# Kernel optimization log

Measured on AMD Instinct MI355X. Metric: run time of the kernel, lower is better.

## Reference

```python
import jax, jax.numpy as jnp
import numpy as np
from jax import lax


def setup_inputs() -> dict:
    key = jax.random.key(0)
    B, S, C = 64, 4096, 128
    timeseries = jax.random.normal(key, (B, S, C), dtype=jnp.float32)
    return {"timeseries": timeseries, "k": 64}


def reference(timeseries, k):
    B, S, C = timeseries.shape
    ffts = jnp.fft.rfft(timeseries, axis=1)          # (B, F, C) complex, F = S//2 + 1
    F = ffts.shape[1]
    mags = jnp.abs(ffts)                              # (B, F, C)
    # top-k magnitudes per (batch, channel): move freq axis last for lax.top_k
    m = jnp.transpose(mags, (0, 2, 1))                # (B, C, F)
    _, idx = lax.top_k(m, k)                          # (B, C, k)
    mask = jnp.zeros((B, C, F), dtype=bool)
    mask = mask.at[jnp.arange(B)[:, None, None],
                   jnp.arange(C)[None, :, None],
                   idx].set(True)
    mask = jnp.transpose(mask, (0, 2, 1))             # (B, F, C)
    filtered = jnp.where(mask, ffts, jnp.zeros((), dtype=ffts.dtype))
    reconstructed = jnp.fft.irfft(filtered, n=S, axis=1)  # (B, S, C) real
    return reconstructed.astype(timeseries.dtype)
```

## Files before the change

### kernel.cpp

```cpp
#include <hip/hip_runtime.h>
#include <math.h>

#define TPB 256
#define SWZ(i) ((i) ^ (((i) >> 5) & 31) ^ ((i) >> 10))

#define A2048 0.0030679615757712823f
#define A256  0.0245436926061702596f
#define A32   0.1963495408493620774f
#define APACK 0.0015339807878856411f
#define EPSB  1.220703125e-4f

__device__ __forceinline__ float2 cadd(float2 a, float2 b){return make_float2(a.x+b.x, a.y+b.y);}
__device__ __forceinline__ float2 csub(float2 a, float2 b){return make_float2(a.x-b.x, a.y-b.y);}
__device__ __forceinline__ float2 cmul(float2 a, float2 b){return make_float2(a.x*b.x-a.y*b.y, a.x*b.y+a.y*b.x);}
__device__ __forceinline__ float2 cni(float2 a){return make_float2(a.y, -a.x);}
__device__ __forceinline__ float2 cpi(float2 a){return make_float2(-a.y, a.x);}

__device__ __forceinline__ int pos2048(int k) {
  return 256*(k&7) + 32*((k>>3)&7) + 4*((k>>6)&7) + ((k>>9)&3);
}

__device__ __forceinline__ void fft8(float2 y[8]) {
  const float S2 = 0.70710678118654752f;
  float2 B0=cadd(y[0],y[4]), B4=csub(y[0],y[4]);
  float2 B1=cadd(y[1],y[5]), B5=csub(y[1],y[5]);
  float2 B2=cadd(y[2],y[6]), B6=csub(y[2],y[6]);
  float2 B3=cadd(y[3],y[7]), B7=csub(y[3],y[7]);
  float2 C0=cadd(B0,B2), C2=csub(B0,B2);
  float2 C1=cadd(B1,B3), C3=csub(B1,B3);
  float2 n6=cni(B6), n7=cni(B7);
  float2 C4=cadd(B4,n6), C6=csub(B4,n6);
  float2 C5=cadd(B5,n7), C7=csub(B5,n7);
  y[0]=cadd(C0,C1); y[4]=csub(C0,C1);
  float2 n3=cni(C3);
  y[2]=cadd(C2,n3); y[6]=csub(C2,n3);
  float2 t5=make_float2(S2*(C5.x+C5.y), S2*(C5.y-C5.x));
  y[1]=cadd(C4,t5); y[5]=csub(C4,t5);
  float2 t7=make_float2(S2*(C7.y-C7.x), -S2*(C7.x+C7.y));
  y[3]=cadd(C6,t7); y[7]=csub(C6,t7);
}

__device__ __forceinline__ void ifft8(float2 y[8]) {
  const float S2 = 0.70710678118654752f;
  float2 B0=cadd(y[0],y[4]), B4=csub(y[0],y[4]);
  float2 B1=cadd(y[1],y[5]), B5=csub(y[1],y[5]);
  float2 B2=cadd(y[2],y[6]), B6=csub(y[2],y[6]);
  float2 B3=cadd(y[3],y[7]), B7=csub(y[3],y[7]);
  float2 C0=cadd(B0,B2), C2=csub(B0,B2);
  float2 C1=cadd(B1,B3), C3=csub(B1,B3);
  float2 p6=cpi(B6), p7=cpi(B7);
  float2 C4=cadd(B4,p6), C6=csub(B4,p6);
  float2 C5=cadd(B5,p7), C7=csub(B5,p7);
  y[0]=cadd(C0,C1); y[4]=csub(C0,C1);
  float2 p3=cpi(C3);
  y[2]=cadd(C2,p3); y[6]=csub(C2,p3);
  float2 t5=make_float2(S2*(C5.x-C5.y), S2*(C5.x+C5.y));
  y[1]=cadd(C4,t5); y[5]=csub(C4,t5);
  float2 t7=make_float2(-S2*(C7.x+C7.y), S2*(C7.x-C7.y));
  y[3]=cadd(C6,t7); y[7]=csub(C6,t7);
}

__device__ __forceinline__ void r8stage(float2* Zf, int idx0, int st, float a1, bool inv) {
  float2 y[8];
#pragma unroll
  for (int s=0;s<8;++s) y[s]=Zf[SWZ(idx0+st*s)];
  float sn, cs; __sincosf(a1, &sn, &cs);
  float2 w1=make_float2(cs,sn);
  float2 w2=cmul(w1,w1), w3=cmul(w2,w1), w4=cmul(w2,w2);
  float2 w5=cmul(w4,w1), w6=cmul(w4,w2), w7=cmul(w4,w3);
  if (inv){
    y[1]=cmul(y[1],w1); y[2]=cmul(y[2],w2); y[3]=cmul(y[3],w3);
    y[4]=cmul(y[4],w4); y[5]=cmul(y[5],w5); y[6]=cmul(y[6],w6); y[7]=cmul(y[7],w7);
    ifft8(y);
  } else {
    fft8(y);
    y[1]=cmul(y[1],w1); y[2]=cmul(y[2],w2); y[3]=cmul(y[3],w3);
    y[4]=cmul(y[4],w4); y[5]=cmul(y[5],w5); y[6]=cmul(y[6],w6); y[7]=cmul(y[7],w7);
  }
#pragma unroll
  for (int s=0;s<8;++s) Zf[SWZ(idx0+st*s)] = y[s];
}

__global__ __launch_bounds__(256) void tposeX(const float* __restrict__ in,
                                              float* __restrict__ out,
                                              int R, int Cd, int lgx) {
  __shared__ float tile[64][65];
  int t = threadIdx.x;
  int q = t & 15, r = t >> 4;
  int id = blockIdx.x;
  int g = id & 7, j = id >> 3;
  int w = ((j >> 3) << 6) | (g << 3) | (j & 7);
  int b = w >> 7;
  int rem = w & 127;
  int gxm = (1 << lgx) - 1;
  int c0 = (rem & gxm) * 64, r0 = (rem >> lgx) * 64;
  const float4* in4 = reinterpret_cast<const float4*>(in + (size_t)b * R * Cd);
  float4* out4 = reinterpret_cast<float4*>(out + (size_t)b * R * Cd);
#pragma unroll
  for (int rr = r; rr < 64; rr += 16) {
    float4 v = in4[((size_t)(r0 + rr) * Cd + c0) / 4 + q];
    tile[rr][4 * q + 0] = v.x; tile[rr][4 * q + 1] = v.y;
    tile[rr][4 * q + 2] = v.z; tile[rr][4 * q + 3] = v.w;
  }
  __syncthreads();
#pragma unroll
  for (int cc = r; cc < 64; cc += 16) {
    float4 wv;
    wv.x = tile[4 * q + 0][cc]; wv.y = tile[4 * q + 1][cc];
    wv.z = tile[4 * q + 2][cc]; wv.w = tile[4 * q + 3][cc];
    out4[((size_t)(c0 + cc) * R + r0) / 4 + q] = wv;
  }
}

__global__ __launch_bounds__(TPB, 6) void fourier_topk_kernel(
    const float* __restrict__ src, float* __restrict__ dst,
    const int* __restrict__ kptr, int strideT) {
  __shared__ float2 Zf[2048];
  __shared__ unsigned int histL[1056];
  __shared__ unsigned char maskA[2052];
  __shared__ int tieIdx[64];
  __shared__ double candV[64];
  __shared__ double cpR[4], cpI[4];
  __shared__ unsigned int bcD, bcR, bcCnt, bcT, bcG, bcTieN;

  const int tid = threadIdx.x;
  int i = blockIdx.x;
  int xj = i & 7, mm = i >> 3;
  int c = 16 * xj + (mm & 15);
  int b = mm >> 4;
  const size_t base = (strideT == 1) ? ((size_t)(b * 128 + c)) * 4096
                                     : ((size_t)b * 4096 * 128 + (size_t)c);
  const float* sp = src + base;
  float* dp = dst + base;

  if (strideT == 1) {
    const float4* sp4 = reinterpret_cast<const float4*>(sp);
#pragma unroll
    for (int it = 0; it < 4; ++it) {
      int t4 = tid + 256 * it;
      float4 v = sp4[t4];
      Zf[SWZ(2*t4)]   = make_float2(v.x, v.y);
      Zf[SWZ(2*t4+1)] = make_float2(v.z, v.w);
    }
  } else {
#pragma unroll
    for (int it = 0; it < 8; ++it) {
      int n = tid + 256 * it;
      float a = sp[(size_t)(2*n) * strideT];
      float bb = sp[(size_t)(2*n+1) * strideT];
      Zf[SWZ(n)] = make_float2(a, bb);
    }
  }
  __syncthreads();

  r8stage(Zf, tid, 256, -A2048 * (float)tid, false);
  __syncthreads();
  r8stage(Zf, 256*(tid>>5) + (tid&31), 32, -A256 * (float)(tid&31), false);
  __syncthreads();
  r8stage(Zf, 32*(tid>>2) + (tid&3), 4, -A32 * (float)(tid&3), false);
  __syncthreads();
#pragma unroll
  for (int h = 0; h < 2; ++h) {
    int i0 = 4 * (tid + 256*h);
    float2 A0=Zf[SWZ(i0)], A1=Zf[SWZ(i0+1)], A2=Zf[SWZ(i0+2)], A3=Zf[SWZ(i0+3)];
    float2 f=cadd(A0,A2), e=csub(A0,A2), g=cadd(A1,A3), d=csub(A1,A3);
    float2 nd=cni(d);
    Zf[SWZ(i0)]   = cadd(f,g);
    Zf[SWZ(i0+1)] = cadd(e,nd);
    Zf[SWZ(i0+2)] = csub(f,g);
    Zf[SWZ(i0+3)] = csub(e,nd);
  }
  __syncthreads();

  float kA[4], kB[4];
#pragma unroll
  for (int jj = 0; jj < 4; ++jj) {
    int k = tid + 256 * jj;
    float2 za = Zf[SWZ(pos2048(k))];
    float2 zb = Zf[SWZ(pos2048((2048 - k) & 2047))];
    float her = 0.5f*(za.x+zb.x), hei = 0.5f*(za.y-zb.y);
    float hor = 0.5f*(za.y+zb.y), hoi = -0.5f*(za.x-zb.x);
    float sn, cs; __sincosf(-APACK * (float)k, &sn, &cs);
    float whr = cs*hor - sn*hoi, whi = cs*hoi + sn*hor;
    float x1r = her + whr, x1i = hei + whi;
    float x2r = her - whr, x2i = whi - hei;
    kA[jj] = x1r*x1r + x1i*x1i;
    kB[jj] = x2r*x2r + x2i*x2i;
  }
  float kNy;
  {
    float2 za = Zf[SWZ(pos2048(1024))];
    kNy = za.x*za.x + za.y*za.y;
  }
  const bool hasNy = (tid == 0);

  int kk = kptr[0];
  if (kk > 2049) kk = 2049;
  if (kk < 1) kk = 1;
  unsigned int prefix = 0u, pmask = 0u, Tkey = 0u;
  bool haveT = false;
  int R = kk;
  unsigned int* myh = &histL[(tid >> 6) * 264];
#pragma unroll 1
  for (int p = 0; p < 4; ++p) {
    if (!haveT) {
      const int sh = 24 - 8 * p;
      for (int idx2 = tid; idx2 < 1056; idx2 += TPB) histL[idx2] = 0u;
      __syncthreads();
#pragma unroll
      for (int jj = 0; jj < 4; ++jj) {
        unsigned int u = __float_as_uint(kA[jj]);
        if ((u & pmask) == prefix) atomicAdd(&myh[(u >> sh) & 255u], 1u);
        u = __float_as_uint(kB[jj]);
        if ((u & pmask) == prefix) atomicAdd(&myh[(u >> sh) & 255u], 1u);
      }
      if (hasNy) {
        unsigned int u = __float_as_uint(kNy);
        if ((u & pmask) == prefix) atomicAdd(&myh[(u >> sh) & 255u], 1u);
      }
      __syncthreads();
      if (tid < 64) {
        int L = tid;
        int s0 = 0, s1 = 0, s2 = 0, s3 = 0;
#pragma unroll
        for (int wv = 0; wv < 4; ++wv) {
          const unsigned int* hw = &histL[wv * 264];
          s0 += (int)hw[4*L]; s1 += (int)hw[4*L+1];
          s2 += (int)hw[4*L+2]; s3 += (int)hw[4*L+3];
        }
        int loc = s0 + s1 + s2 + s3;
        int suf = loc;
#pragma unroll
        for (int off = 1; off < 64; off <<= 1) {
          int tt = __shfl(suf, (L + off) & 63, 64);
          suf += (L + off < 64) ? tt : 0;
        }
        int e3 = suf - loc, i3 = e3 + s3;
        int e2 = i3,        i2 = e2 + s2;
        int e1 = i2,        i1 = e1 + s1;
        int e0 = i1,        i0 = e0 + s0;
        if (e3 < R && R <= i3) { bcD = 4*L+3; bcR = R - e3; bcCnt = s3; }
        if (e2 < R && R <= i2) { bcD = 4*L+2; bcR = R - e2; bcCnt = s2; }
        if (e1 < R && R <= i1) { bcD = 4*L+1; bcR = R - e1; bcCnt = s1; }
        if (e0 < R && R <= i0) { bcD = 4*L+0; bcR = R - e0; bcCnt = s0; }
      }
      __syncthreads();
      prefix |= (bcD << sh);
      pmask |= (255u << sh);
      R = (int)bcR;
      if (bcCnt == 1u) {
#pragma unroll
        for (int jj = 0; jj < 4; ++jj) {
          unsigned int u = __float_as_uint(kA[jj]);
          if ((u & pmask) == prefix) bcT = u;
          u = __float_as_uint(kB[jj]);
          if ((u & pmask) == prefix) bcT = u;
        }
        if (hasNy) {
          unsigned int u = __float_as_uint(kNy);
          if ((u & pmask) == prefix) bcT = u;
        }
        __syncthreads();
        Tkey = bcT;
        haveT = true;
      }
      __syncthreads();
    }
  }
  if (!haveT) Tkey = prefix;

  float Tf = __uint_as_float(Tkey);
  float Thi = Tf * (1.0f + EPSB), Tlo = Tf * (1.0f - EPSB);
  if (tid == 0) { bcG = 0u; bcTieN = 0u; }
  __syncthreads();
#pragma unroll
  for (int jj = 0; jj < 4; ++jj) {
    float v = kA[jj];
    if (v > Thi) atomicAdd(&bcG, 1u);
    else if (v >= Tlo) {
      int pos = (int)atomicAdd(&bcTieN, 1u);
      if (pos < 64) tieIdx[pos] = tid + 256 * jj;
    }
    v = kB[jj];
    if (v > Thi) atomicAdd(&bcG, 1u);
    else if (v >= Tlo) {
      int pos = (int)atomicAdd(&bcTieN, 1u);
      if (pos < 64) tieIdx[pos] = 2048 - (tid + 256 * jj);
    }
  }
  if (hasNy) {
    if (kNy > Thi) atomicAdd(&bcG, 1u);
    else if (kNy >= Tlo) {
      int pos = (int)atomicAdd(&bcTieN, 1u);
      if (pos < 64) tieIdx[pos] = 1024;
    }
  }
  __syncthreads();
  int G = (int)bcG, E = (int)bcTieN, need = kk - G;

  if (need >= E) {
#pragma unroll
    for (int jj = 0; jj < 4; ++jj) {
      int k = tid + 256 * jj;
      maskA[k]        = (kA[jj] >= Tlo) ? 1 : 0;
      maskA[2048 - k] = (kB[jj] >= Tlo) ? 1 : 0;
    }
    if (hasNy) maskA[1024] = (kNy >= Tlo) ? 1 : 0;
    __syncthreads();
  } else {
#pragma unroll
    for (int jj = 0; jj < 4; ++jj) {
      int k = tid + 256 * jj;
      maskA[k]        = (kA[jj] > Thi) ? 1 : 0;
      maskA[2048 - k] = (kB[jj] > Thi) ? 1 : 0;
    }
    if (hasNy) maskA[1024] = (kNy > Thi) ? 1 : 0;
    __syncthreads();
    int nt = E < 64 ? E : 64;
    for (int ci = 0; ci < nt; ++ci) {
      int kq = tieIdx[ci];
      double sr = 0.0, si = 0.0;
#pragma unroll 1
      for (int j = 0; j < 16; ++j) {
        int m = tid + 256 * j;
        double xm = (double)sp[(size_t)m * strideT];
        int a = (kq * m) & 4095;
        double ang = 1.5339807878856412e-3 * (double)a;
        double sv, cv; sincos(ang, &sv, &cv);
        sr += xm * cv; si -= xm * sv;
      }
#pragma unroll
      for (int off = 1; off < 64; off <<= 1) {
        sr += __shfl_xor(sr, off); si += __shfl_xor(si, off);
      }
      if ((tid & 63) == 0) { cpR[tid >> 6] = sr; cpI[tid >> 6] = si; }
      __syncthreads();
      if (tid == 0) {
        double Rr = cpR[0]+cpR[1]+cpR[2]+cpR[3];
        double Ii = cpI[0]+cpI[1]+cpI[2]+cpI[3];
        candV[ci] = Rr*Rr + Ii*Ii;
      }
      __syncthreads();
    }
    if (tid == 0) {
      unsigned char* ch = (unsigned char*)histL;
      for (int t = 0; t < nt; ++t) ch[t] = 0;
      int lim = need < nt ? need : nt;
      for (int s = 0; s < lim; ++s) {
        int best = -1;
        for (int t = 0; t < nt; ++t) {
          if (ch[t]) continue;
          if (best < 0 || candV[t] > candV[best] ||
              (candV[t] == candV[best] && tieIdx[t] < tieIdx[best])) best = t;
        }
        if (best >= 0) { ch[best] = 1; maskA[tieIdx[best]] = 1; }
      }
    }
    __syncthreads();
  }

#pragma unroll
  for (int jj = 0; jj < 4; ++jj) {
    int k = tid + 256 * jj;
    if (k == 0) {
      int p0 = SWZ(pos2048(0));
      float2 z0 = Zf[p0];
      float X0 = z0.x + z0.y, XN = z0.x - z0.y;
      float A = maskA[0] ? X0 : 0.0f, Bv = maskA[2048] ? XN : 0.0f;
      Zf[p0] = make_float2(0.5f*(A + Bv), 0.5f*(A - Bv));
      int p1 = SWZ(pos2048(1024));
      float2 z1 = Zf[p1];
      float m1 = maskA[1024] ? 1.0f : 0.0f;
      Zf[p1] = make_float2(m1 * z1.x, m1 * z1.y);
    } else {
      int pa = SWZ(pos2048(k)), pb = SWZ(pos2048(2048 - k));
      float2 za = Zf[pa], zb = Zf[pb];
      float her = 0.5f*(za.x+zb.x), hei = 0.5f*(za.y-zb.y);
      float hor = 0.5f*(za.y+zb.y), hoi = -0.5f*(za.x-zb.x);
      float sn, cs; __sincosf(-APACK * (float)k, &sn, &cs);
      float wr = cs, wi = sn;
      float whr = wr*hor - wi*hoi, whi = wr*hoi + wi*hor;
      float x1r = her + whr, x1i = hei + whi;
      float x2r = her - whr, x2i = whi - hei;
      float mA = maskA[k] ? 1.0f : 0.0f, mB = maskA[2048 - k] ? 1.0f : 0.0f;
      float Ar = mA*x1r, Ai = mA*x1i, Br = mB*x2r, Bi = mB*x2i;
      float sr = Ar + Br, si = Ai - Bi;
      float dr = Ar - Br, di = Ai + Bi;
      float tr = wr*dr + wi*di, ti = wr*di - wi*dr;
      Zf[pa] = make_float2(0.5f*(sr - ti), 0.5f*(si + tr));
      Zf[pb] = make_float2(0.5f*(sr + ti), 0.5f*(tr - si));
    }
  }
  __syncthreads();

#pragma unroll
  for (int h = 0; h < 2; ++h) {
    int i0 = 4 * (tid + 256*h);
    float2 y0=Zf[SWZ(i0)], y1=Zf[SWZ(i0+1)], y2=Zf[SWZ(i0+2)], y3=Zf[SWZ(i0+3)];
    float2 f=cadd(y0,y2), e=csub(y0,y2), g=cadd(y1,y3), d=csub(y1,y3);
    float2 pd=cpi(d);
    Zf[SWZ(i0)]   = cadd(f,g);
    Zf[SWZ(i0+1)] = cadd(e,pd);
    Zf[SWZ(i0+2)] = csub(f,g);
    Zf[SWZ(i0+3)] = csub(e,pd);
  }
  __syncthreads();
  r8stage(Zf, 32*(tid>>2) + (tid&3), 4, A32 * (float)(tid&3), true);
  __syncthreads();
  r8stage(Zf, 256*(tid>>5) + (tid&31), 32, A256 * (float)(tid&31), true);
  __syncthreads();
  r8stage(Zf, tid, 256, A2048 * (float)tid, true);
  __syncthreads();

  const float scf = 1.0f / 2048.0f;
  if (strideT == 1) {
    float4* dp4 = reinterpret_cast<float4*>(dp);
#pragma unroll
    for (int it = 0; it < 4; ++it) {
      int t4 = tid + 256 * it;
      float2 v0 = Zf[SWZ(2*t4)], v1 = Zf[SWZ(2*t4+1)];
      dp4[t4] = make_float4(v0.x*scf, v0.y*scf, v1.x*scf, v1.y*scf);
    }
  } else {
#pragma unroll
    for (int it = 0; it < 8; ++it) {
      int n = tid + 256 * it;
      float2 v = Zf[SWZ(n)];
      dp[(size_t)(2*n) * strideT]   = v.x * scf;
      dp[(size_t)(2*n+1) * strideT] = v.y * scf;
    }
  }
}

extern "C" void kernel_launch(void* const* d_in, const int* in_sizes, int n_in,
                              void* d_out, int out_size, void* d_ws, size_t ws_size,
                              hipStream_t stream) {
  (void)in_sizes; (void)n_in; (void)out_size;
  const float* ts = (const float*)d_in[0];
  const int* kptr = (const int*)d_in[1];
  float* out = (float*)d_out;
  float* ws = (float*)d_ws;
  const int B = 64, S = 4096, C = 128;
  const size_t sigBytes = (size_t)B * S * C * sizeof(float);

  if (ws_size >= sigBytes) {
    tposeX<<<8192, 256, 0, stream>>>(ts, ws, S, C, 1);
    fourier_topk_kernel<<<B * C, TPB, 0, stream>>>(ws, ws, kptr, 1);
    tposeX<<<8192, 256, 0, stream>>>(ws, out, C, S, 6);
  } else {
    fourier_topk_kernel<<<B * C, TPB, 0, stream>>>(ts, out, kptr, C);
  }
}
```

Baseline: 437.6 us.

## Drop transpose kernels and read strided input directly with channel-grouped block mapping

Removes the two transpose passes through workspace and always runs the FFT/top-k kernel on the original (B,S,C) layout with strided per-channel loads and stores. The block-to-(batch,channel) mapping is reworked so consecutive blocks cover 32 adjacent channels of the same batch, which lets strided accesses share cache lines across concurrently running blocks. The mask array is aliased onto the histogram buffer to cut shared memory, and the occupancy hint drops from 6 to 4 blocks per CU. This saves two full read/write passes over the signal, at the cost of uncoalesced 4-byte strided global accesses that depend on L2 reuse across blocks.

```diff
diff --git a/kernel.cpp b/kernel.cpp
--- a/kernel.cpp
+++ b/kernel.cpp
@@ -81,53 +81,23 @@
   for (int s=0;s<8;++s) Zf[SWZ(idx0+st*s)] = y[s];
 }
 
-__global__ __launch_bounds__(256) void tposeX(const float* __restrict__ in,
-                                              float* __restrict__ out,
-                                              int R, int Cd, int lgx) {
-  __shared__ float tile[64][65];
-  int t = threadIdx.x;
-  int q = t & 15, r = t >> 4;
-  int id = blockIdx.x;
-  int g = id & 7, j = id >> 3;
-  int w = ((j >> 3) << 6) | (g << 3) | (j & 7);
-  int b = w >> 7;
-  int rem = w & 127;
-  int gxm = (1 << lgx) - 1;
-  int c0 = (rem & gxm) * 64, r0 = (rem >> lgx) * 64;
-  const float4* in4 = reinterpret_cast<const float4*>(in + (size_t)b * R * Cd);
-  float4* out4 = reinterpret_cast<float4*>(out + (size_t)b * R * Cd);
-#pragma unroll
-  for (int rr = r; rr < 64; rr += 16) {
-    float4 v = in4[((size_t)(r0 + rr) * Cd + c0) / 4 + q];
-    tile[rr][4 * q + 0] = v.x; tile[rr][4 * q + 1] = v.y;
-    tile[rr][4 * q + 2] = v.z; tile[rr][4 * q + 3] = v.w;
-  }
-  __syncthreads();
-#pragma unroll
-  for (int cc = r; cc < 64; cc += 16) {
-    float4 wv;
-    wv.x = tile[4 * q + 0][cc]; wv.y = tile[4 * q + 1][cc];
-    wv.z = tile[4 * q + 2][cc]; wv.w = tile[4 * q + 3][cc];
-    out4[((size_t)(c0 + cc) * R + r0) / 4 + q] = wv;
-  }
-}
-
-__global__ __launch_bounds__(TPB, 6) void fourier_topk_kernel(
+__global__ __launch_bounds__(TPB, 4) void fourier_topk_kernel(
     const float* __restrict__ src, float* __restrict__ dst,
     const int* __restrict__ kptr, int strideT) {
   __shared__ float2 Zf[2048];
   __shared__ unsigned int histL[1056];
-  __shared__ unsigned char maskA[2052];
   __shared__ int tieIdx[64];
   __shared__ double candV[64];
-  __shared__ double cpR[4], cpI[4];
+  __shared__ double cpRI[8];
   __shared__ unsigned int bcD, bcR, bcCnt, bcT, bcG, bcTieN;
+  unsigned char* maskA = reinterpret_cast<unsigned char*>(histL);
 
   const int tid = threadIdx.x;
   int i = blockIdx.x;
-  int xj = i & 7, mm = i >> 3;
-  int c = 16 * xj + (mm & 15);
-  int b = mm >> 4;
+  int x = i & 7, j = i >> 3;
+  int g = x + 8 * (j >> 5);
+  int b = g >> 2;
+  int c = 32 * (g & 3) + (j & 31);
   const size_t base = (strideT == 1) ? ((size_t)(b * 128 + c)) * 4096
                                      : ((size_t)b * 4096 * 128 + (size_t)c);
   const float* sp = src + base;
@@ -163,11 +133,11 @@
   for (int h = 0; h < 2; ++h) {
     int i0 = 4 * (tid + 256*h);
     float2 A0=Zf[SWZ(i0)], A1=Zf[SWZ(i0+1)], A2=Zf[SWZ(i0+2)], A3=Zf[SWZ(i0+3)];
-    float2 f=cadd(A0,A2), e=csub(A0,A2), g=cadd(A1,A3), d=csub(A1,A3);
+    float2 f=cadd(A0,A2), e=csub(A0,A2), g2=cadd(A1,A3), d=csub(A1,A3);
     float2 nd=cni(d);
-    Zf[SWZ(i0)]   = cadd(f,g);
+    Zf[SWZ(i0)]   = cadd(f,g2);
     Zf[SWZ(i0+1)] = cadd(e,nd);
-    Zf[SWZ(i0+2)] = csub(f,g);
+    Zf[SWZ(i0+2)] = csub(f,g2);
     Zf[SWZ(i0+3)] = csub(e,nd);
   }
   __syncthreads();
@@ -321,8 +291,8 @@
       int kq = tieIdx[ci];
       double sr = 0.0, si = 0.0;
 #pragma unroll 1
-      for (int j = 0; j < 16; ++j) {
-        int m = tid + 256 * j;
+      for (int jq = 0; jq < 16; ++jq) {
+        int m = tid + 256 * jq;
         double xm = (double)sp[(size_t)m * strideT];
         int a = (kq * m) & 4095;
         double ang = 1.5339807878856412e-3 * (double)a;
@@ -333,17 +303,17 @@
       for (int off = 1; off < 64; off <<= 1) {
         sr += __shfl_xor(sr, off); si += __shfl_xor(si, off);
       }
-      if ((tid & 63) == 0) { cpR[tid >> 6] = sr; cpI[tid >> 6] = si; }
+      if ((tid & 63) == 0) { cpRI[tid >> 6] = sr; cpRI[4 + (tid >> 6)] = si; }
       __syncthreads();
       if (tid == 0) {
-        double Rr = cpR[0]+cpR[1]+cpR[2]+cpR[3];
-        double Ii = cpI[0]+cpI[1]+cpI[2]+cpI[3];
+        double Rr = cpRI[0]+cpRI[1]+cpRI[2]+cpRI[3];
+        double Ii = cpRI[4]+cpRI[5]+cpRI[6]+cpRI[7];
         candV[ci] = Rr*Rr + Ii*Ii;
       }
       __syncthreads();
     }
     if (tid == 0) {
-      unsigned char* ch = (unsigned char*)histL;
+      unsigned char* ch = reinterpret_cast<unsigned char*>(cpRI);
       for (int t = 0; t < nt; ++t) ch[t] = 0;
       int lim = need < nt ? need : nt;
       for (int s = 0; s < lim; ++s) {
@@ -397,11 +367,11 @@
   for (int h = 0; h < 2; ++h) {
     int i0 = 4 * (tid + 256*h);
     float2 y0=Zf[SWZ(i0)], y1=Zf[SWZ(i0+1)], y2=Zf[SWZ(i0+2)], y3=Zf[SWZ(i0+3)];
-    float2 f=cadd(y0,y2), e=csub(y0,y2), g=cadd(y1,y3), d=csub(y1,y3);
+    float2 f=cadd(y0,y2), e=csub(y0,y2), g2=cadd(y1,y3), d=csub(y1,y3);
     float2 pd=cpi(d);
-    Zf[SWZ(i0)]   = cadd(f,g);
+    Zf[SWZ(i0)]   = cadd(f,g2);
     Zf[SWZ(i0+1)] = cadd(e,pd);
-    Zf[SWZ(i0+2)] = csub(f,g);
+    Zf[SWZ(i0+2)] = csub(f,g2);
     Zf[SWZ(i0+3)] = csub(e,pd);
   }
   __syncthreads();
@@ -435,19 +405,11 @@
 extern "C" void kernel_launch(void* const* d_in, const int* in_sizes, int n_in,
                               void* d_out, int out_size, void* d_ws, size_t ws_size,
                               hipStream_t stream) {
-  (void)in_sizes; (void)n_in; (void)out_size;
+  (void)in_sizes; (void)n_in; (void)out_size; (void)d_ws; (void)ws_size;
   const float* ts = (const float*)d_in[0];
   const int* kptr = (const int*)d_in[1];
   float* out = (float*)d_out;
-  float* ws = (float*)d_ws;
-  const int B = 64, S = 4096, C = 128;
-  const size_t sigBytes = (size_t)B * S * C * sizeof(float);
-
-  if (ws_size >= sigBytes) {
-    tposeX<<<8192, 256, 0, stream>>>(ts, ws, S, C, 1);
-    fourier_topk_kernel<<<B * C, TPB, 0, stream>>>(ws, ws, kptr, 1);
-    tposeX<<<8192, 256, 0, stream>>>(ws, out, C, S, 6);
-  } else {
-    fourier_topk_kernel<<<B * C, TPB, 0, stream>>>(ts, out, kptr, C);
-  }
-}
+  const int B = 64, C = 128;
+
+  fourier_topk_kernel<<<B * C, TPB, 0, stream>>>(ts, out, kptr, C);
+}
```

After: 470.9 us. +7.6%, slower.
